# Kernel tuning notes

Measured on AMD Instinct MI355X. Metric: run time of the kernel, lower is better.

Reference implementation:

```python
import jax, jax.numpy as jnp
import numpy as np

B = 131072
E = 768       # embedding_dim
T = 3         # tree_dim
D = E + T     # fused dim = 771
H = 96        # hidden_dim
C = 3         # num_classes

def setup_inputs() -> dict:
    key = jax.random.key(0)
    k1, k2, k3, k4 = jax.random.split(key, 4)
    embeddings = jax.random.normal(k1, (B, E), dtype=jnp.float32)
    tree_probs = jax.random.uniform(k2, (B, T), dtype=jnp.float32)
    # LayerNorm params
    ln_gamma = jnp.ones((D,), dtype=jnp.float32)
    ln_beta = jnp.zeros((D,), dtype=jnp.float32)
    # Linear layers (torch nn.Linear: y = x @ W.T + b); store as [in, out]
    w1 = jax.random.normal(k3, (D, H), dtype=jnp.float32) * (1.0 / np.sqrt(D))
    b1 = jnp.zeros((H,), dtype=jnp.float32)
    w2 = jax.random.normal(k4, (H, C), dtype=jnp.float32) * (1.0 / np.sqrt(H))
    b2 = jnp.zeros((C,), dtype=jnp.float32)
    return {"embeddings": embeddings, "tree_probs": tree_probs,
            "ln_gamma": ln_gamma, "ln_beta": ln_beta,
            "w1": w1, "b1": b1, "w2": w2, "b2": b2}

def reference(embeddings, tree_probs, ln_gamma, ln_beta, w1, b1, w2, b2):
    # concat + LayerNorm + Linear-GELU-(Dropout eval=identity)-Linear
    fused = jnp.concatenate([embeddings, tree_probs], axis=1)  # [B, D]
    mu = jnp.mean(fused, axis=-1, keepdims=True)
    var = jnp.mean(jnp.square(fused - mu), axis=-1, keepdims=True)
    x = (fused - mu) * jax.lax.rsqrt(var + 1e-5) * ln_gamma + ln_beta
    h = jax.nn.gelu(x @ w1 + b1, approximate=False)  # torch GELU default = exact erf
    return h @ w2 + b2  # [B, C]
```

## Files before the change

kernel.cpp:

```cpp
#include <hip/hip_runtime.h>
#include <hip/hip_fp16.h>
#include <math.h>


typedef _Float16 half8 __attribute__((ext_vector_type(8)));
typedef float floatx4 __attribute__((ext_vector_type(4)));

#define E_DIM 768
#define D_DIM 771
#define H_DIM 96
#define KSTEPS 25
#define WB_ELEMS (KSTEPS * 6 * 64 * 8)

__global__ void pack_w1(const float* __restrict__ w1, const float* __restrict__ gamma,
                        _Float16* __restrict__ wB) {
    int idx = blockIdx.x * 256 + threadIdx.x;
    int j = idx & 7;
    int l = (idx >> 3) & 63;
    int tn = idx >> 9;
    int t = tn / 6;
    int n0 = tn - t * 6;
    int k = t * 32 + ((l >> 4) << 3) + j;
    int n = n0 * 16 + (l & 15);
    float v = 0.f;
    if (k < D_DIM) v = w1[k * H_DIM + n] * gamma[k];
    wB[idx] = (_Float16)v;
}

__global__ void make_b1p(const float* __restrict__ w1, const float* __restrict__ beta,
                         const float* __restrict__ b1, float* __restrict__ b1p) {
    int n = blockIdx.x;
    int l = threadIdx.x;
    float acc = 0.f;
    for (int k = l; k < D_DIM; k += 64)
        acc += beta[k] * w1[k * H_DIM + n];
#pragma unroll
    for (int d = 1; d < 64; d <<= 1)
        acc += __shfl_xor(acc, d, 64);
    if (l == 0) b1p[n] = acc + b1[n];
}

__global__ __launch_bounds__(256) void fusion_main(
    const float* __restrict__ emb, const float* __restrict__ tp,
    const _Float16* __restrict__ wB, const float* __restrict__ b1p,
    const float* __restrict__ w2, const float* __restrict__ b2,
    float* __restrict__ out)
{
    const int lane = threadIdx.x & 63;
    const int wv = threadIdx.x >> 6;
    const int m = lane & 15;
    const int q = lane >> 4;
    const int rowBase = blockIdx.x * 64 + wv * 16;
    const long r = (long)(rowBase + m);
    const float* erow = emb + r * (long)E_DIM;

    half8 areg[KSTEPS];
    float sum0 = 0.f, sum1 = 0.f, ss0 = 0.f, ss1 = 0.f;
#pragma unroll
    for (int t = 0; t < 24; ++t) {
        floatx4 x0 = *(const floatx4*)(erow + t * 32 + q * 8);
        floatx4 x1 = *(const floatx4*)(erow + t * 32 + q * 8 + 4);
        sum0 += (x0.x + x0.y) + (x0.z + x0.w);
        sum1 += (x1.x + x1.y) + (x1.z + x1.w);
        ss0 += x0.x * x0.x; ss0 += x0.y * x0.y; ss0 += x0.z * x0.z; ss0 += x0.w * x0.w;
        ss1 += x1.x * x1.x; ss1 += x1.y * x1.y; ss1 += x1.z * x1.z; ss1 += x1.w * x1.w;
        half8 a;
        a[0] = (_Float16)x0.x; a[1] = (_Float16)x0.y; a[2] = (_Float16)x0.z; a[3] = (_Float16)x0.w;
        a[4] = (_Float16)x1.x; a[5] = (_Float16)x1.y; a[6] = (_Float16)x1.z; a[7] = (_Float16)x1.w;
        areg[t] = a;
    }
    {
        float v0 = 0.f, v1 = 0.f, v2 = 0.f;
        if (q == 0) {
            const float* tpr = tp + r * 3;
            v0 = tpr[0]; v1 = tpr[1]; v2 = tpr[2];
        }
        sum0 += (v0 + v1) + v2;
        ss0 += v0 * v0; ss0 += v1 * v1; ss0 += v2 * v2;
        half8 a = {(_Float16)v0, (_Float16)v1, (_Float16)v2,
                   (_Float16)0.f, (_Float16)0.f, (_Float16)0.f, (_Float16)0.f, (_Float16)0.f};
        areg[24] = a;
    }

    float sum = (sum0 + sum1), ss = (ss0 + ss1);
    sum += __shfl_xor(sum, 16, 64);  ss += __shfl_xor(ss, 16, 64);
    sum += __shfl_xor(sum, 32, 64);  ss += __shfl_xor(ss, 32, 64);
    const float inv_n = 1.0f / 771.0f;
    float mean = sum * inv_n;
    float var = ss * inv_n - mean * mean;
    float sc = rsqrtf(var + 1e-5f);
    float off = -mean * sc;

    const _Float16 sh = (_Float16)sc;
    const _Float16 ch = (_Float16)off;
#pragma unroll
    for (int t = 0; t < KSTEPS; ++t)
        areg[t] = areg[t] * sh + ch;

    const half8* __restrict__ wB8 = (const half8*)wB;
    floatx4 acc[6];
#pragma unroll
    for (int n0 = 0; n0 < 6; ++n0) acc[n0] = (floatx4){0.f, 0.f, 0.f, 0.f};
#pragma unroll
    for (int t = 0; t < KSTEPS; ++t) {
#pragma unroll
        for (int n0 = 0; n0 < 6; ++n0) {
            half8 b = wB8[(t * 6 + n0) * 64 + lane];
            acc[n0] = __builtin_amdgcn_mfma_f32_16x16x32_f16(areg[t], b, acc[n0], 0, 0, 0);
        }
    }

    float b1v[6];
    float w2v[6][3];
#pragma unroll
    for (int n0 = 0; n0 < 6; ++n0) {
        int n = n0 * 16 + m;
        b1v[n0] = b1p[n];
        w2v[n0][0] = w2[n * 3 + 0];
        w2v[n0][1] = w2[n * 3 + 1];
        w2v[n0][2] = w2[n * 3 + 2];
    }
    const float kInvSqrt2 = 0.70710678118654752f;
#pragma unroll
    for (int reg = 0; reg < 4; ++reg) {
        float r0 = 0.f, r1 = 0.f, r2 = 0.f;
#pragma unroll
        for (int n0 = 0; n0 < 6; ++n0) {
            float h = acc[n0][reg] + b1v[n0];
            h = 0.5f * h * (1.0f + erff(h * kInvSqrt2));
            r0 += h * w2v[n0][0];
            r1 += h * w2v[n0][1];
            r2 += h * w2v[n0][2];
        }
#pragma unroll
        for (int d = 1; d < 16; d <<= 1) {
            r0 += __shfl_xor(r0, d, 64);
            r1 += __shfl_xor(r1, d, 64);
            r2 += __shfl_xor(r2, d, 64);
        }
        if (m == 0) {
            long row = (long)rowBase + q * 4 + reg;
            out[row * 3 + 0] = r0 + b2[0];
            out[row * 3 + 1] = r1 + b2[1];
            out[row * 3 + 2] = r2 + b2[2];
        }
    }
}

extern "C" void kernel_launch(void* const* d_in, const int* in_sizes, int n_in,
                              void* d_out, int out_size, void* d_ws, size_t ws_size,
                              hipStream_t stream) {
    const float* emb   = (const float*)d_in[0];
    const float* tp    = (const float*)d_in[1];
    const float* gamma = (const float*)d_in[2];
    const float* beta  = (const float*)d_in[3];
    const float* w1    = (const float*)d_in[4];
    const float* b1    = (const float*)d_in[5];
    const float* w2    = (const float*)d_in[6];
    const float* b2    = (const float*)d_in[7];
    float* out = (float*)d_out;

    _Float16* wB = (_Float16*)d_ws;
    float* b1p = (float*)((char*)d_ws + WB_ELEMS * sizeof(_Float16));

    hipLaunchKernelGGL(pack_w1, dim3(WB_ELEMS / 256), dim3(256), 0, stream, w1, gamma, wB);
    hipLaunchKernelGGL(make_b1p, dim3(H_DIM), dim3(64), 0, stream, w1, beta, b1, b1p);
    hipLaunchKernelGGL(fusion_main, dim3(131072 / 64), dim3(256), 0, stream,
                       emb, tp, wB, b1p, w2, b2, out);
}
```

Measured before the change: 678.1 us.

## Fold LayerNorm into post-GEMM epilogue so MFMA streams with loads

LayerNorm is moved algebraically to after the GEMM: raw fp16 inputs go into the MFMAs as they are loaded, and the result is corrected per row with sc*(acc - mean*colsum(gamma*W1)) + b1'. This removes the 25-register A buffer and the normalize pass, so the matrix work can overlap with the global loads and register pressure drops. The cost is a precomputed column-sum vector, per-row shuffles in the epilogue, and a possible accuracy loss because unnormalized values are cast to fp16 and mean cancellation now happens in fp32 after the GEMM.

```diff
diff --git a/kernel.cpp b/kernel.cpp
--- a/kernel.cpp
+++ b/kernel.cpp
@@ -27,22 +27,29 @@
     wB[idx] = (_Float16)v;
 }
 
-__global__ void make_b1p(const float* __restrict__ w1, const float* __restrict__ beta,
-                         const float* __restrict__ b1, float* __restrict__ b1p) {
+__global__ void make_vecs(const float* __restrict__ w1, const float* __restrict__ gamma,
+                          const float* __restrict__ beta, const float* __restrict__ b1,
+                          float* __restrict__ b1p, float* __restrict__ colsum) {
     int n = blockIdx.x;
     int l = threadIdx.x;
-    float acc = 0.f;
-    for (int k = l; k < D_DIM; k += 64)
-        acc += beta[k] * w1[k * H_DIM + n];
+    float accb = 0.f, accg = 0.f;
+    for (int k = l; k < D_DIM; k += 64) {
+        float w = w1[k * H_DIM + n];
+        accb += beta[k] * w;
+        accg += gamma[k] * w;
+    }
 #pragma unroll
-    for (int d = 1; d < 64; d <<= 1)
-        acc += __shfl_xor(acc, d, 64);
-    if (l == 0) b1p[n] = acc + b1[n];
+    for (int d = 1; d < 64; d <<= 1) {
+        accb += __shfl_xor(accb, d, 64);
+        accg += __shfl_xor(accg, d, 64);
+    }
+    if (l == 0) { b1p[n] = accb + b1[n]; colsum[n] = accg; }
 }
 
 __global__ __launch_bounds__(256) void fusion_main(
     const float* __restrict__ emb, const float* __restrict__ tp,
     const _Float16* __restrict__ wB, const float* __restrict__ b1p,
+    const float* __restrict__ colsum,
     const float* __restrict__ w2, const float* __restrict__ b2,
     float* __restrict__ out)
 {
@@ -53,21 +60,27 @@
     const int rowBase = blockIdx.x * 64 + wv * 16;
     const long r = (long)(rowBase + m);
     const float* erow = emb + r * (long)E_DIM;
+    const half8* __restrict__ wB8 = (const half8*)wB;
 
-    half8 areg[KSTEPS];
-    float sum0 = 0.f, sum1 = 0.f, ss0 = 0.f, ss1 = 0.f;
+    floatx4 acc[6];
+#pragma unroll
+    for (int n0 = 0; n0 < 6; ++n0) acc[n0] = (floatx4){0.f, 0.f, 0.f, 0.f};
+
+    float sum = 0.f, ss = 0.f;
 #pragma unroll
     for (int t = 0; t < 24; ++t) {
         floatx4 x0 = *(const floatx4*)(erow + t * 32 + q * 8);
         floatx4 x1 = *(const floatx4*)(erow + t * 32 + q * 8 + 4);
-        sum0 += (x0.x + x0.y) + (x0.z + x0.w);
-        sum1 += (x1.x + x1.y) + (x1.z + x1.w);
-        ss0 += x0.x * x0.x; ss0 += x0.y * x0.y; ss0 += x0.z * x0.z; ss0 += x0.w * x0.w;
-        ss1 += x1.x * x1.x; ss1 += x1.y * x1.y; ss1 += x1.z * x1.z; ss1 += x1.w * x1.w;
+        sum += (x0.x + x0.y) + (x0.z + x0.w);
+        sum += (x1.x + x1.y) + (x1.z + x1.w);
+        ss += x0.x * x0.x; ss += x0.y * x0.y; ss += x0.z * x0.z; ss += x0.w * x0.w;
+        ss += x1.x * x1.x; ss += x1.y * x1.y; ss += x1.z * x1.z; ss += x1.w * x1.w;
         half8 a;
         a[0] = (_Float16)x0.x; a[1] = (_Float16)x0.y; a[2] = (_Float16)x0.z; a[3] = (_Float16)x0.w;
         a[4] = (_Float16)x1.x; a[5] = (_Float16)x1.y; a[6] = (_Float16)x1.z; a[7] = (_Float16)x1.w;
-        areg[t] = a;
+#pragma unroll
+        for (int n0 = 0; n0 < 6; ++n0)
+            acc[n0] = __builtin_amdgcn_mfma_f32_16x16x32_f16(a, wB8[(t * 6 + n0) * 64 + lane], acc[n0], 0, 0, 0);
     }
     {
         float v0 = 0.f, v1 = 0.f, v2 = 0.f;
@@ -75,47 +88,28 @@
             const float* tpr = tp + r * 3;
             v0 = tpr[0]; v1 = tpr[1]; v2 = tpr[2];
         }
-        sum0 += (v0 + v1) + v2;
-        ss0 += v0 * v0; ss0 += v1 * v1; ss0 += v2 * v2;
+        sum += (v0 + v1) + v2;
+        ss += v0 * v0; ss += v1 * v1; ss += v2 * v2;
         half8 a = {(_Float16)v0, (_Float16)v1, (_Float16)v2,
                    (_Float16)0.f, (_Float16)0.f, (_Float16)0.f, (_Float16)0.f, (_Float16)0.f};
-        areg[24] = a;
+#pragma unroll
+        for (int n0 = 0; n0 < 6; ++n0)
+            acc[n0] = __builtin_amdgcn_mfma_f32_16x16x32_f16(a, wB8[(24 * 6 + n0) * 64 + lane], acc[n0], 0, 0, 0);
     }
 
-    float sum = (sum0 + sum1), ss = (ss0 + ss1);
     sum += __shfl_xor(sum, 16, 64);  ss += __shfl_xor(ss, 16, 64);
     sum += __shfl_xor(sum, 32, 64);  ss += __shfl_xor(ss, 32, 64);
     const float inv_n = 1.0f / 771.0f;
     float mean = sum * inv_n;
     float var = ss * inv_n - mean * mean;
     float sc = rsqrtf(var + 1e-5f);
-    float off = -mean * sc;
 
-    const _Float16 sh = (_Float16)sc;
-    const _Float16 ch = (_Float16)off;
-#pragma unroll
-    for (int t = 0; t < KSTEPS; ++t)
-        areg[t] = areg[t] * sh + ch;
-
-    const half8* __restrict__ wB8 = (const half8*)wB;
-    floatx4 acc[6];
-#pragma unroll
-    for (int n0 = 0; n0 < 6; ++n0) acc[n0] = (floatx4){0.f, 0.f, 0.f, 0.f};
-#pragma unroll
-    for (int t = 0; t < KSTEPS; ++t) {
-#pragma unroll
-        for (int n0 = 0; n0 < 6; ++n0) {
-            half8 b = wB8[(t * 6 + n0) * 64 + lane];
-            acc[n0] = __builtin_amdgcn_mfma_f32_16x16x32_f16(areg[t], b, acc[n0], 0, 0, 0);
-        }
-    }
-
-    float b1v[6];
-    float w2v[6][3];
+    float b1v[6], csv[6], w2v[6][3];
 #pragma unroll
     for (int n0 = 0; n0 < 6; ++n0) {
         int n = n0 * 16 + m;
         b1v[n0] = b1p[n];
+        csv[n0] = colsum[n];
         w2v[n0][0] = w2[n * 3 + 0];
         w2v[n0][1] = w2[n * 3 + 1];
         w2v[n0][2] = w2[n * 3 + 2];
@@ -123,10 +117,13 @@
     const float kInvSqrt2 = 0.70710678118654752f;
 #pragma unroll
     for (int reg = 0; reg < 4; ++reg) {
+        int row = q * 4 + reg;
+        float mu_r = __shfl(mean, row, 64);
+        float sc_r = __shfl(sc, row, 64);
         float r0 = 0.f, r1 = 0.f, r2 = 0.f;
 #pragma unroll
         for (int n0 = 0; n0 < 6; ++n0) {
-            float h = acc[n0][reg] + b1v[n0];
+            float h = sc_r * (acc[n0][reg] - mu_r * csv[n0]) + b1v[n0];
             h = 0.5f * h * (1.0f + erff(h * kInvSqrt2));
             r0 += h * w2v[n0][0];
             r1 += h * w2v[n0][1];
@@ -139,10 +136,10 @@
             r2 += __shfl_xor(r2, d, 64);
         }
         if (m == 0) {
-            long row = (long)rowBase + q * 4 + reg;
-            out[row * 3 + 0] = r0 + b2[0];
-            out[row * 3 + 1] = r1 + b2[1];
-            out[row * 3 + 2] = r2 + b2[2];
+            long orow = (long)rowBase + row;
+            out[orow * 3 + 0] = r0 + b2[0];
+            out[orow * 3 + 1] = r1 + b2[1];
+            out[orow * 3 + 2] = r2 + b2[2];
         }
     }
 }
@@ -161,10 +158,11 @@
     float* out = (float*)d_out;
 
     _Float16* wB = (_Float16*)d_ws;
-    float* b1p = (float*)((char*)d_ws + WB_ELEMS * sizeof(_Float16));
+    float* b1p    = (float*)((char*)d_ws + WB_ELEMS * sizeof(_Float16));
+    float* colsum = b1p + H_DIM;
 
     hipLaunchKernelGGL(pack_w1, dim3(WB_ELEMS / 256), dim3(256), 0, stream, w1, gamma, wB);
-    hipLaunchKernelGGL(make_b1p, dim3(H_DIM), dim3(64), 0, stream, w1, beta, b1, b1p);
+    hipLaunchKernelGGL(make_vecs, dim3(H_DIM), dim3(64), 0, stream, w1, gamma, beta, b1, b1p, colsum);
     hipLaunchKernelGGL(fusion_main, dim3(131072 / 64), dim3(256), 0, stream,
-                       emb, tp, wB, b1p, w2, b2, out);
+                       emb, tp, wB, b1p, colsum, w2, b2, out);
 }
```

New measurement: 637.9 us. 5.9% less time.
